# Performance work log

Hardware: AMD Instinct MI355X
Metric: run time of the kernel (lower is better)

The kernel has to match this reference:

```python
import jax, jax.numpy as jnp
import numpy as np

N_NODES = 50000

def setup_inputs() -> dict:
    key = jax.random.key(0)
    k1, k2, k3, k4, k5 = jax.random.split(key, 5)
    x = jax.random.normal(k1, (50000, 512), dtype=jnp.float32)
    edge_row = jax.random.randint(k2, (800000,), 0, N_NODES, dtype=jnp.int64)
    edge_col = jax.random.randint(k3, (800000,), 0, N_NODES, dtype=jnp.int64)
    edge_val = jax.random.uniform(k4, (800000,), dtype=jnp.float32)
    # init like torch: uniform(-stdv, stdv), stdv = 1/sqrt(out_features)
    stdv = 1.0 / np.sqrt(96.0)
    weight = jax.random.uniform(k5, (512, 96), minval=-stdv, maxval=stdv, dtype=jnp.float32)
    return {"x": x, "edge_row": edge_row, "edge_col": edge_col, "edge_val": edge_val, "weight": weight}

def reference(x, edge_row, edge_col, edge_val, weight):
    # support = X @ W  -- dense GEMM [N, F_in] x [F_in, F_out]
    support = x @ weight
    # sparse adjacency matmul: out[row] += val * support[col]
    msgs = edge_val[:, None] * support[edge_col]          # [E, F_out]
    out = jax.ops.segment_sum(msgs, edge_row, num_segments=N_NODES)
    # act = ReLU (module default); bias=False
    return jax.nn.relu(out)
```

## Files before the change

kernel.cpp:

```cpp
#include <hip/hip_runtime.h>

#define N_NODES 50000
#define F_IN    512
#define F_OUT   96
#define N_EDGES 800000

#define RPB    128
#define NBKT   391
#define CAP    2560
#define ECHUNK 4096
#define NCHUNK ((N_EDGES + ECHUNK - 1) / ECHUNK)
#define GEMM_BLOCKS ((N_NODES + 127) / 128)

typedef __attribute__((ext_vector_type(8))) short bf16x8;
typedef __attribute__((ext_vector_type(4))) float f32x4;

__device__ __forceinline__ unsigned short f2bf(float f) {
    unsigned int u = __float_as_uint(f);
    unsigned int r = (u + 0x7FFFu + ((u >> 16) & 1u)) >> 16;
    return (unsigned short)r;
}
__device__ __forceinline__ float bf2f(unsigned short h) {
    return __uint_as_float(((unsigned int)h) << 16);
}

__global__ __launch_bounds__(256) void k_wcast(const float* __restrict__ w,
                                               unsigned short* __restrict__ wTq,
                                               int* __restrict__ bcnt) {
    if (blockIdx.x == 0) {
        const int t = threadIdx.x;
        bcnt[t] = 0;
        if (t < 144) bcnt[256 + t] = 0;
    }
    const int i = blockIdx.x * 256 + threadIdx.x;
    if (i < F_OUT * F_IN) {
        const int j    = i & 7;
        const int lane = (i >> 3) & 63;
        const int ks   = (i >> 9) & 1;
        const int tp   = i >> 10;
        const int t    = tp % 6;
        const int p    = tp / 6;
        const int lr   = lane & 15;
        const int kg   = lane >> 4;
        const int n    = t * 16 + lr;
        const int k    = p * 64 + ks * 32 + kg * 8 + j;
        wTq[i] = f2bf(w[(size_t)k * F_OUT + n]);
    }
}

__global__ __launch_bounds__(512) void k_fused(const float* __restrict__ x,
                                               const unsigned short* __restrict__ wTq,
                                               unsigned short* __restrict__ support,
                                               const int* __restrict__ erow,
                                               const int* __restrict__ ecol,
                                               const float* __restrict__ eval,
                                               int* __restrict__ bcnt,
                                               float2* __restrict__ bucket) {
    __shared__ int smem[1200];
    const int tid = threadIdx.x;

    if (blockIdx.x < NCHUNK) {
        int* hist  = smem;
        int* gbase = smem + 400;
        int* lcur  = smem + 800;
        for (int i = tid; i < NBKT; i += 512) { hist[i] = 0; lcur[i] = 0; }
        __syncthreads();

        const int base = blockIdx.x * ECHUNK;
        const int n = min(ECHUNK, N_EDGES - base);

        for (int i = tid; i < n; i += 512)
            atomicAdd(&hist[erow[base + i] >> 7], 1);
        __syncthreads();

        for (int b = tid; b < NBKT; b += 512)
            gbase[b] = hist[b] ? atomicAdd(&bcnt[b], hist[b]) : 0;
        __syncthreads();

        for (int i = tid; i < n; i += 512) {
            const int r = erow[base + i];
            const int b = r >> 7;
            const int pos = gbase[b] + atomicAdd(&lcur[b], 1);
            if (pos >= 0 && pos < CAP)
                bucket[(size_t)b * CAP + pos] = make_float2(
                    __int_as_float(((r & 127) << 16) | ecol[base + i]),
                    eval[base + i]);
        }
        return;
    }

    const int lane = tid & 63;
    const int wave = tid >> 6;
    const int lr   = lane & 15;
    const int kg   = lane >> 4;

    const int wrow0 = (blockIdx.x - NCHUNK) * 128 + wave * 16;
    int grow = wrow0 + lr;
    if (grow > N_NODES - 1) grow = N_NODES - 1;
    const float* aptr = x + (size_t)grow * F_IN + kg * 8;
    const unsigned short* bb = wTq + lane * 8;

    f32x4 acc[6];
    #pragma unroll
    for (int t = 0; t < 6; ++t) acc[t] = (f32x4){0.f, 0.f, 0.f, 0.f};

    #pragma unroll
    for (int p = 0; p < 8; ++p) {
        #pragma unroll
        for (int ks = 0; ks < 2; ++ks) {
            const float* a = aptr + p * 64 + ks * 32;
            const float4 a0 = *reinterpret_cast<const float4*>(a);
            const float4 a1 = *reinterpret_cast<const float4*>(a + 4);
            bf16x8 af;
            af[0] = (short)f2bf(a0.x); af[1] = (short)f2bf(a0.y);
            af[2] = (short)f2bf(a0.z); af[3] = (short)f2bf(a0.w);
            af[4] = (short)f2bf(a1.x); af[5] = (short)f2bf(a1.y);
            af[6] = (short)f2bf(a1.z); af[7] = (short)f2bf(a1.w);
            #pragma unroll
            for (int t = 0; t < 6; ++t) {
                const int frag = p * 12 + t * 2 + ks;
                const bf16x8 bq = *reinterpret_cast<const bf16x8*>(bb + (size_t)frag * 512);
                acc[t] = __builtin_amdgcn_mfma_f32_16x16x32_bf16(af, bq, acc[t], 0, 0, 0);
            }
        }
    }

    #pragma unroll
    for (int t = 0; t < 6; ++t) {
        #pragma unroll
        for (int r = 0; r < 4; ++r) {
            const int row = wrow0 + kg * 4 + r;
            if (row < N_NODES)
                support[(size_t)row * F_OUT + t * 16 + lr] = f2bf(acc[t][r]);
        }
    }
}

__global__ __launch_bounds__(256) void kS_sort(const int* __restrict__ bcnt,
                                               const float2* __restrict__ bucket,
                                               float2* __restrict__ bucket2,
                                               int* __restrict__ rowOffs) {
    __shared__ int cnt[RPB];
    __shared__ int sc[RPB];
    __shared__ int rbase[RPB];
    __shared__ int rcur[RPB];
    const int b   = blockIdx.x;
    const int tid = threadIdx.x;

    if (tid < RPB) { cnt[tid] = 0; rcur[tid] = 0; }
    __syncthreads();

    const int beg = b * CAP;
    const int n   = min(bcnt[b], CAP);

    for (int i = tid; i < n; i += 256)
        atomicAdd(&cnt[(__float_as_int(bucket[beg + i].x) >> 16) & 127], 1);
    __syncthreads();

    if (tid < RPB) sc[tid] = cnt[tid];
    __syncthreads();
    #pragma unroll
    for (int off = 1; off < RPB; off <<= 1) {
        int a = 0;
        if (tid < RPB && tid >= off) a = sc[tid - off];
        __syncthreads();
        if (tid < RPB) sc[tid] += a;
        __syncthreads();
    }
    if (tid < RPB) {
        const int rb = beg + sc[tid] - cnt[tid];
        rbase[tid] = rb;
        rowOffs[b * 129 + tid] = rb;
    }
    if (tid == RPB) rowOffs[b * 129 + RPB] = beg + n;
    __syncthreads();

    for (int i = tid; i < n; i += 256) {
        const float2 ev  = bucket[beg + i];
        const int    key = __float_as_int(ev.x);
        const int    r   = (key >> 16) & 127;
        const int    pos = rbase[r] + atomicAdd(&rcur[r], 1);
        bucket2[pos] = make_float2(__int_as_float(key & 0xFFFF), ev.y);
    }
}

__global__ __launch_bounds__(256) void k_gather(const int* __restrict__ rowOffs,
                                                const float2* __restrict__ bucket2,
                                                const unsigned short* __restrict__ support,
                                                float* __restrict__ out) {
    const int gid = blockIdx.x * 256 + threadIdx.x;
    if (gid >= N_NODES * 6) return;
    const int r   = gid / 6;
    const int f16 = gid - r * 6;

    const int idx = (r >> 7) * 129 + (r & 127);
    const int beg = rowOffs[idx];
    const int end = rowOffs[idx + 1];

    float acc[16];
    #pragma unroll
    for (int j = 0; j < 16; ++j) acc[j] = 0.f;

    for (int i = beg; i < end; ++i) {
        const float2 cv = bucket2[i];
        const int   c = __float_as_int(cv.x);
        const float v = cv.y;
        const unsigned short* sp = support + (size_t)c * F_OUT + f16 * 16;
        const bf16x8 s0 = *reinterpret_cast<const bf16x8*>(sp);
        const bf16x8 s1 = *reinterpret_cast<const bf16x8*>(sp + 8);
        #pragma unroll
        for (int j = 0; j < 8; ++j) {
            acc[j]     = fmaf(v, bf2f((unsigned short)s0[j]), acc[j]);
            acc[8 + j] = fmaf(v, bf2f((unsigned short)s1[j]), acc[8 + j]);
        }
    }

    float* o = out + (size_t)r * F_OUT + f16 * 16;
    #pragma unroll
    for (int q = 0; q < 4; ++q) {
        float4 ov;
        ov.x = fmaxf(acc[q * 4 + 0], 0.f);
        ov.y = fmaxf(acc[q * 4 + 1], 0.f);
        ov.z = fmaxf(acc[q * 4 + 2], 0.f);
        ov.w = fmaxf(acc[q * 4 + 3], 0.f);
        *reinterpret_cast<float4*>(o + q * 4) = ov;
    }
}

extern "C" void kernel_launch(void* const* d_in, const int* in_sizes, int n_in,
                              void* d_out, int out_size, void* d_ws, size_t ws_size,
                              hipStream_t stream) {
    const float* x    = (const float*)d_in[0];
    const int*   erow = (const int*)d_in[1];
    const int*   ecol = (const int*)d_in[2];
    const float* eval = (const float*)d_in[3];
    const float* w    = (const float*)d_in[4];
    float*       out  = (float*)d_out;

    unsigned short* support = (unsigned short*)d_ws;
    int*    bcnt    = (int*)((char*)d_ws + 9600000);
    int*    rowOffs = bcnt + 400;
    unsigned short* wTq = (unsigned short*)(rowOffs + 50560);
    float2* bucket  = (float2*)((char*)wTq + 98304);
    float2* bucket2 = bucket + (size_t)NBKT * CAP;

    k_wcast<<<(F_OUT * F_IN + 255) / 256, 256, 0, stream>>>(w, wTq, bcnt);

    k_fused<<<NCHUNK + GEMM_BLOCKS, 512, 0, stream>>>(x, wTq, support,
                                                      erow, ecol, eval,
                                                      bcnt, bucket);

    kS_sort<<<NBKT, 256, 0, stream>>>(bcnt, bucket, bucket2, rowOffs);

    const int gthreads = N_NODES * 6;
    k_gather<<<(gthreads + 255) / 256, 256, 0, stream>>>(rowOffs, bucket2, support, out);
}
```

Baseline: 87.97 us.

## Split GEMM into LDS-staged async-load kernel and fuse weight cast with bucketing

Moves the X@W GEMM into its own kernel, with one 64-thread wave per 16 rows. The kernel stages all of its A rows and double-buffered B panels into LDS through global_load_lds, using an XOR swizzle and explicit vmcnt waits to overlap loads with MFMA. The weight cast now runs inside the edge-bucketing kernel, and the counter zeroing moves to a tiny separate kernel. This raises the launch count to five and forces the GEMM to wait on the bucketing kernel instead of running alongside it, trading that concurrency for better memory-level parallelism in the GEMM.

```diff
diff --git a/kernel.cpp b/kernel.cpp
--- a/kernel.cpp
+++ b/kernel.cpp
@@ -10,10 +10,25 @@
 #define CAP    2560
 #define ECHUNK 4096
 #define NCHUNK ((N_EDGES + ECHUNK - 1) / ECHUNK)
-#define GEMM_BLOCKS ((N_NODES + 127) / 128)
+#define WCB    96
+#define GEMM_BLOCKS (N_NODES / 16)
 
 typedef __attribute__((ext_vector_type(8))) short bf16x8;
 typedef __attribute__((ext_vector_type(4))) float f32x4;
+
+typedef const __attribute__((address_space(1))) void* gas_ptr;
+typedef __attribute__((address_space(3))) void* las_ptr;
+
+__device__ __forceinline__ void gload_lds16(const void* g, void* l) {
+    __builtin_amdgcn_global_load_lds((gas_ptr)g, (las_ptr)l, 16, 0, 0);
+}
+
+#define VMCNT_SB(n) do { \
+    asm volatile("s_waitcnt vmcnt(" #n ")" ::: "memory"); \
+    __builtin_amdgcn_sched_barrier(0); \
+} while (0)
+
+#define PIN __builtin_amdgcn_sched_barrier(0)
 
 __device__ __forceinline__ unsigned short f2bf(float f) {
     unsigned int u = __float_as_uint(f);
@@ -24,93 +39,111 @@
     return __uint_as_float(((unsigned int)h) << 16);
 }
 
-__global__ __launch_bounds__(256) void k_wcast(const float* __restrict__ w,
-                                               unsigned short* __restrict__ wTq,
-                                               int* __restrict__ bcnt) {
-    if (blockIdx.x == 0) {
-        const int t = threadIdx.x;
-        bcnt[t] = 0;
-        if (t < 144) bcnt[256 + t] = 0;
-    }
-    const int i = blockIdx.x * 256 + threadIdx.x;
-    if (i < F_OUT * F_IN) {
-        const int j    = i & 7;
-        const int lane = (i >> 3) & 63;
-        const int ks   = (i >> 9) & 1;
-        const int tp   = i >> 10;
-        const int t    = tp % 6;
-        const int p    = tp / 6;
-        const int lr   = lane & 15;
-        const int kg   = lane >> 4;
-        const int n    = t * 16 + lr;
-        const int k    = p * 64 + ks * 32 + kg * 8 + j;
-        wTq[i] = f2bf(w[(size_t)k * F_OUT + n]);
-    }
-}
-
-__global__ __launch_bounds__(512) void k_fused(const float* __restrict__ x,
-                                               const unsigned short* __restrict__ wTq,
-                                               unsigned short* __restrict__ support,
-                                               const int* __restrict__ erow,
-                                               const int* __restrict__ ecol,
-                                               const float* __restrict__ eval,
-                                               int* __restrict__ bcnt,
-                                               float2* __restrict__ bucket) {
+__global__ __launch_bounds__(512) void k_zero(int* __restrict__ bcnt) {
+    if (threadIdx.x < 400) bcnt[threadIdx.x] = 0;
+}
+
+__global__ __launch_bounds__(512) void k_fillwcast(const int* __restrict__ erow,
+                                                   const int* __restrict__ ecol,
+                                                   const float* __restrict__ eval,
+                                                   int* __restrict__ bcnt,
+                                                   float2* __restrict__ bucket,
+                                                   const float* __restrict__ w,
+                                                   unsigned short* __restrict__ wTq) {
     __shared__ int smem[1200];
     const int tid = threadIdx.x;
 
-    if (blockIdx.x < NCHUNK) {
-        int* hist  = smem;
-        int* gbase = smem + 400;
-        int* lcur  = smem + 800;
-        for (int i = tid; i < NBKT; i += 512) { hist[i] = 0; lcur[i] = 0; }
-        __syncthreads();
-
-        const int base = blockIdx.x * ECHUNK;
-        const int n = min(ECHUNK, N_EDGES - base);
-
-        for (int i = tid; i < n; i += 512)
-            atomicAdd(&hist[erow[base + i] >> 7], 1);
-        __syncthreads();
-
-        for (int b = tid; b < NBKT; b += 512)
-            gbase[b] = hist[b] ? atomicAdd(&bcnt[b], hist[b]) : 0;
-        __syncthreads();
-
-        for (int i = tid; i < n; i += 512) {
-            const int r = erow[base + i];
-            const int b = r >> 7;
-            const int pos = gbase[b] + atomicAdd(&lcur[b], 1);
-            if (pos >= 0 && pos < CAP)
-                bucket[(size_t)b * CAP + pos] = make_float2(
-                    __int_as_float(((r & 127) << 16) | ecol[base + i]),
-                    eval[base + i]);
+    if (blockIdx.x >= NCHUNK) {
+        const int i = (blockIdx.x - NCHUNK) * 512 + tid;
+        if (i < F_OUT * F_IN) {
+            const int j    = i & 7;
+            const int lane = (i >> 3) & 63;
+            const int ks   = (i >> 9) & 1;
+            const int tp   = i >> 10;
+            const int t    = tp % 6;
+            const int p    = tp / 6;
+            const int lr   = lane & 15;
+            const int kg   = lane >> 4;
+            const int n    = t * 16 + lr;
+            const int k    = p * 64 + ks * 32 + kg * 8 + j;
+            wTq[i] = f2bf(w[(size_t)k * F_OUT + n]);
         }
         return;
     }
 
-    const int lane = tid & 63;
-    const int wave = tid >> 6;
-    const int lr   = lane & 15;
-    const int kg   = lane >> 4;
-
-    const int wrow0 = (blockIdx.x - NCHUNK) * 128 + wave * 16;
-    int grow = wrow0 + lr;
-    if (grow > N_NODES - 1) grow = N_NODES - 1;
-    const float* aptr = x + (size_t)grow * F_IN + kg * 8;
-    const unsigned short* bb = wTq + lane * 8;
+    int* hist  = smem;
+    int* gbase = smem + 400;
+    int* lcur  = smem + 800;
+    for (int i = tid; i < NBKT; i += 512) { hist[i] = 0; lcur[i] = 0; }
+    __syncthreads();
+
+    const int base = blockIdx.x * ECHUNK;
+    const int n = min(ECHUNK, N_EDGES - base);
+
+    for (int i = tid; i < n; i += 512)
+        atomicAdd(&hist[erow[base + i] >> 7], 1);
+    __syncthreads();
+
+    for (int b = tid; b < NBKT; b += 512)
+        gbase[b] = hist[b] ? atomicAdd(&bcnt[b], hist[b]) : 0;
+    __syncthreads();
+
+    for (int i = tid; i < n; i += 512) {
+        const int r = erow[base + i];
+        const int b = r >> 7;
+        const int pos = gbase[b] + atomicAdd(&lcur[b], 1);
+        if (pos >= 0 && pos < CAP)
+            bucket[(size_t)b * CAP + pos] = make_float2(
+                __int_as_float(((r & 127) << 16) | ecol[base + i]),
+                eval[base + i]);
+    }
+}
+
+__global__ __launch_bounds__(64, 1) void k_gemm(const float* __restrict__ x,
+                                                const unsigned short* __restrict__ wTq,
+                                                unsigned short* __restrict__ support) {
+    __shared__ __align__(16) char sA[32768];
+    __shared__ __align__(16) char sB[24576];
+
+    const int tid = threadIdx.x;
+    const int lr  = tid & 15;
+    const int kg  = tid >> 4;
+    const int r0  = blockIdx.x * 16;
 
     f32x4 acc[6];
     #pragma unroll
     for (int t = 0; t < 6; ++t) acc[t] = (f32x4){0.f, 0.f, 0.f, 0.f};
 
-    #pragma unroll
-    for (int p = 0; p < 8; ++p) {
+    auto BSTAGE = [&](int slot, int p) {
+        const unsigned short* src = wTq + (size_t)p * 6144;
+        char* dst = sB + slot * 12288;
+        #pragma unroll
+        for (int i = 0; i < 12; ++i)
+            gload_lds16(src + i * 512 + tid * 8, dst + i * 1024 + tid * 16);
+    };
+
+    auto ASTAGE_ALL = [&]() {
+        #pragma unroll
+        for (int i = 0; i < 32; ++i) {
+            const int chunk = i * 64 + tid;
+            const int p     = chunk >> 8;
+            const int local = chunk & 255;
+            const int row   = local >> 4;
+            const int s16   = local & 15;
+            gload_lds16(x + (size_t)(r0 + row) * F_IN + p * 64 + ((s16 ^ row) << 2),
+                        sA + chunk * 16);
+        }
+    };
+
+    auto COMPUTE = [&](int p) {
+        const char* pa = sA + p * 4096;
+        const char* pb = sB + (p & 1) * 12288;
         #pragma unroll
         for (int ks = 0; ks < 2; ++ks) {
-            const float* a = aptr + p * 64 + ks * 32;
-            const float4 a0 = *reinterpret_cast<const float4*>(a);
-            const float4 a1 = *reinterpret_cast<const float4*>(a + 4);
+            const int s0 = (ks * 8 + kg * 2)     ^ lr;
+            const int s1 = (ks * 8 + kg * 2 + 1) ^ lr;
+            const float4 a0 = *reinterpret_cast<const float4*>(pa + lr * 256 + s0 * 16);
+            const float4 a1 = *reinterpret_cast<const float4*>(pa + lr * 256 + s1 * 16);
             bf16x8 af;
             af[0] = (short)f2bf(a0.x); af[1] = (short)f2bf(a0.y);
             af[2] = (short)f2bf(a0.z); af[3] = (short)f2bf(a0.w);
@@ -118,18 +151,31 @@
             af[6] = (short)f2bf(a1.z); af[7] = (short)f2bf(a1.w);
             #pragma unroll
             for (int t = 0; t < 6; ++t) {
-                const int frag = p * 12 + t * 2 + ks;
-                const bf16x8 bq = *reinterpret_cast<const bf16x8*>(bb + (size_t)frag * 512);
+                const bf16x8 bq = *reinterpret_cast<const bf16x8*>(
+                    pb + (t * 2 + ks) * 1024 + tid * 16);
                 acc[t] = __builtin_amdgcn_mfma_f32_16x16x32_bf16(af, bq, acc[t], 0, 0, 0);
             }
         }
-    }
+    };
+
+    BSTAGE(0, 0);  PIN;
+    BSTAGE(1, 1);  PIN;
+    ASTAGE_ALL();  PIN;
+
+    VMCNT_SB(28); COMPUTE(0); BSTAGE(0, 2); PIN;
+    VMCNT_SB(36); COMPUTE(1); BSTAGE(1, 3); PIN;
+    VMCNT_SB(12); COMPUTE(2); BSTAGE(0, 4); PIN;
+    VMCNT_SB(12); COMPUTE(3); BSTAGE(1, 5); PIN;
+    VMCNT_SB(12); COMPUTE(4); BSTAGE(0, 6); PIN;
+    VMCNT_SB(12); COMPUTE(5); BSTAGE(1, 7); PIN;
+    VMCNT_SB(12); COMPUTE(6);
+    VMCNT_SB(0);  COMPUTE(7);
 
     #pragma unroll
     for (int t = 0; t < 6; ++t) {
         #pragma unroll
         for (int r = 0; r < 4; ++r) {
-            const int row = wrow0 + kg * 4 + r;
+            const int row = r0 + kg * 4 + r;
             if (row < N_NODES)
                 support[(size_t)row * F_OUT + t * 16 + lr] = f2bf(acc[t][r]);
         }
@@ -244,11 +290,12 @@
     float2* bucket  = (float2*)((char*)wTq + 98304);
     float2* bucket2 = bucket + (size_t)NBKT * CAP;
 
-    k_wcast<<<(F_OUT * F_IN + 255) / 256, 256, 0, stream>>>(w, wTq, bcnt);
-
-    k_fused<<<NCHUNK + GEMM_BLOCKS, 512, 0, stream>>>(x, wTq, support,
-                                                      erow, ecol, eval,
-                                                      bcnt, bucket);
+    k_zero<<<1, 512, 0, stream>>>(bcnt);
+
+    k_fillwcast<<<NCHUNK + WCB, 512, 0, stream>>>(erow, ecol, eval,
+                                                  bcnt, bucket, w, wTq);
+
+    k_gemm<<<GEMM_BLOCKS, 64, 0, stream>>>(x, wTq, support);
 
     kS_sort<<<NBKT, 256, 0, stream>>>(bcnt, bucket, bucket2, rowOffs);
 
```

Measured after the change: 114.4 us. 1.3x slower.
